# Performance work log

Hardware: AMD Instinct MI355X
Metric: run time of the kernel (lower is better)

## Reference

```python
import jax, jax.numpy as jnp
import numpy as np

B, E, H, W, HEADS = 2, 128, 64, 64, 4
FUSED = 2 * E + 1          # concat fusion: C_state + C_trigger + 1 (gnn context)
FC = FUSED // 2            # 128 fusion output channels (= AttentionMIL feature_dim)
EPS = 1e-5
NEG = -1e9


def _conv(x, w, b=None, pad=0):
    out = jax.lax.conv_general_dilated(x, w, (1, 1), [(pad, pad), (pad, pad)],
                                       dimension_numbers=('NCHW', 'OIHW', 'NCHW'))
    return out if b is None else out + b[None, :, None, None]


def _bn(x, g, b):
    # training-mode batchnorm (batch statistics), matching torch default mode
    m = x.mean((0, 2, 3), keepdims=True)
    v = x.var((0, 2, 3), keepdims=True)
    return g[None, :, None, None] * (x - m) * jax.lax.rsqrt(v + EPS) + b[None, :, None, None]


def _mha(q_in, kv_in, w_qkv, b_qkv, w_out, b_out, nheads):
    Bq, L, Em = q_in.shape
    d = Em // nheads
    wq, wk, wv = jnp.split(w_qkv, 3, axis=0)
    bq, bk, bv = jnp.split(b_qkv, 3, axis=0)
    q = (q_in @ wq.T + bq).reshape(Bq, L, nheads, d)
    k = (kv_in @ wk.T + bk).reshape(Bq, -1, nheads, d)
    v = (kv_in @ wv.T + bv).reshape(Bq, -1, nheads, d)
    scores = jnp.einsum('bqhd,bkhd->bhqk', q, k) / jnp.sqrt(jnp.asarray(d, q.dtype))
    attn = jax.nn.softmax(scores, axis=-1)
    out = jnp.einsum('bhqk,bkhd->bqhd', attn, v).reshape(Bq, L, Em)
    return out @ w_out.T + b_out


def setup_inputs() -> dict:
    key = jax.random.key(0)
    ks = jax.random.split(key, 24)
    n = lambda k, s: jax.random.normal(k, s, jnp.float32)
    p = lambda k, s: 0.02 * jax.random.normal(k, s, jnp.float32)
    return dict(
        state_features=n(ks[0], (B, E, H, W)),
        trigger_features=n(ks[1], (B, E, H, W)),
        gnn_context=n(ks[2], (B, 1, H, W)),
        zone_patches=jax.random.randint(ks[3], (B, H, W), 0, 16).astype(jnp.int32),
        cats=jax.random.randint(ks[4], (B,), 0, 16).astype(jnp.int32),
        labels=jax.random.uniform(ks[5], (B,), jnp.float32),
        s2t_qkv_w=p(ks[6], (3 * E, E)), s2t_qkv_b=p(ks[7], (3 * E,)),
        s2t_out_w=p(ks[8], (E, E)), s2t_out_b=p(ks[9], (E,)),
        t2s_qkv_w=p(ks[10], (3 * E, E)), t2s_qkv_b=p(ks[11], (3 * E,)),
        t2s_out_w=p(ks[12], (E, E)), t2s_out_b=p(ks[13], (E,)),
        fconv1_w=p(ks[14], (FC, FUSED, 3, 3)),
        fbn1_g=jnp.ones((FC,), jnp.float32), fbn1_b=jnp.zeros((FC,), jnp.float32),
        fconv2_w=p(ks[15], (FC, FC, 3, 3)),
        fbn2_g=jnp.ones((FC,), jnp.float32), fbn2_b=jnp.zeros((FC,), jnp.float32),
        outc_w=p(ks[16], (1, FC, 1, 1)), outc_b=p(ks[17], (1,)),
        attn1_w=p(ks[18], (128, FC, 1, 1)), attn1_b=p(ks[19], (128,)),
        attn2_w=p(ks[20], (1, 128, 1, 1)), attn2_b=p(ks[21], (1,)),
    )


def reference(state_features, trigger_features, gnn_context, zone_patches, cats, labels,
              s2t_qkv_w, s2t_qkv_b, s2t_out_w, s2t_out_b,
              t2s_qkv_w, t2s_qkv_b, t2s_out_w, t2s_out_b,
              fconv1_w, fbn1_g, fbn1_b, fconv2_w, fbn2_g, fbn2_b,
              outc_w, outc_b, attn1_w, attn1_b, attn2_w, attn2_b):
    Bs = state_features.shape[0]
    # ---- CrossAttentionFusion ----
    sf = state_features.reshape(Bs, E, H * W).transpose(0, 2, 1)    # (B, HW, E)
    tf = trigger_features.reshape(Bs, E, H * W).transpose(0, 2, 1)
    s2t = _mha(sf, tf, s2t_qkv_w, s2t_qkv_b, s2t_out_w, s2t_out_b, HEADS)
    t2s = _mha(tf, sf, t2s_qkv_w, t2s_qkv_b, t2s_out_w, t2s_out_b, HEADS)
    s2t = s2t.transpose(0, 2, 1).reshape(Bs, E, H, W)
    t2s = t2s.transpose(0, 2, 1).reshape(Bs, E, H, W)
    fused = jnp.concatenate([s2t, t2s, gnn_context], axis=1)        # (B, 257, H, W)
    x = jax.nn.relu(_bn(_conv(fused, fconv1_w, pad=1), fbn1_g, fbn1_b))
    feat = jax.nn.relu(_bn(_conv(x, fconv2_w, pad=1), fbn2_g, fbn2_b))  # (B, FC, H, W)
    # ---- pixel logit head (decoder outc) ----
    pixel_logits = _conv(feat, outc_w, outc_b)[:, 0]                # (B, H, W)
    # ---- AttentionMIL (vectorized over batch) ----
    a = jax.nn.relu(_conv(feat, attn1_w, attn1_b))
    scores = _conv(a, attn2_w, attn2_b)[:, 0]                       # (B, H, W)
    mask = (zone_patches == cats[:, None, None]) & (zone_patches > 0)
    has = mask.any((1, 2))
    masked = jnp.where(mask, scores, NEG)                           # score*1 on valid, -1e9 elsewhere
    wts = jax.nn.softmax(masked.reshape(Bs, -1), axis=-1).reshape(Bs, H, W)
    attention_maps = jnp.where(has[:, None, None], wts, 0.0)
    bag = (pixel_logits * wts * mask.astype(wts.dtype)).sum((1, 2))
    bag = jnp.where(has, bag, 0.0)
    # BCEWithLogitsLoss(mean): softplus(x) - x*y
    loss = jnp.mean(jax.nn.softplus(bag) - bag * labels)
    return loss, attention_maps
```

## Files before the change

kernel.cpp:

```cpp
#include <hip/hip_runtime.h>
#include <hip/hip_bf16.h>
#include <math.h>

#define L 4096
#define ECH 128
#define BCH 2
#define NHEAD 4
#define FUSEDC 257
#define CPAD 288

typedef __attribute__((ext_vector_type(8))) short bs8;
typedef __attribute__((ext_vector_type(4))) short bs4;
typedef __attribute__((ext_vector_type(4))) float fx4;

#define SCL 0.25503518f

static __device__ __forceinline__ short f2bfs(float x) {
  unsigned u = __float_as_uint(x);
  u += 0x7fffu + ((u >> 16) & 1u);
  return (short)(u >> 16);
}

static __device__ __forceinline__ float bf2f(short s) {
  return __uint_as_float((unsigned)(unsigned short)s << 16);
}

static __device__ __forceinline__ float exp2a(float x) {
  float r; asm("v_exp_f32 %0, %1" : "=v"(r) : "v"(x)); return r;
}

static __device__ __forceinline__ unsigned pk2(float lo, float hi) {
  unsigned r; asm("v_cvt_pk_bf16_f32 %0, %1, %2" : "=v"(r) : "v"(lo), "v"(hi)); return r;
}

__global__ void prep_fused(const float* __restrict__ c1w, const float* __restrict__ c2w,
                           const float* __restrict__ wS, const float* __restrict__ wT,
                           const float* __restrict__ woS, const float* __restrict__ woT,
                           const float* __restrict__ sf, const float* __restrict__ tf,
                           short* __restrict__ W1b, short* __restrict__ W2b,
                           short* __restrict__ wSb, short* __restrict__ wTb,
                           short* __restrict__ woSb, short* __restrict__ woTb,
                           short* __restrict__ Xs, short* __restrict__ Xt) {
  __shared__ float t[32][33];
  int bid = blockIdx.x;
  if (bid < 2064) {
    int i = bid * 256 + threadIdx.x;
    if (i < 331776) {
      int ci = i % CPAD; int rest = i / CPAD; int co = rest & 127; int tap = rest >> 7;
      W1b[i] = (ci < FUSEDC) ? f2bfs(c1w[(co * FUSEDC + ci) * 9 + tap]) : (short)0;
    } else if (i < 479232) {
      int j = i - 331776;
      int ci = j & 127; int co = (j >> 7) & 127; int tap = j >> 14;
      W2b[j] = f2bfs(c2w[(co * 128 + ci) * 9 + tap]);
    } else {
      int k = i - 479232;
      float s = (k < 16384) ? SCL : 1.0f;
      wSb[k] = f2bfs(wS[k] * s);
      wTb[k] = f2bfs(wT[k] * s);
      if (k < 16384) {
        woSb[k] = f2bfs(woS[k]);
        woTb[k] = f2bfs(woT[k]);
      }
    }
  } else {
    int id = bid - 2064;
    int bx = (id & 127) * 32;
    int by = ((id >> 7) & 3) * 32;
    int z = id >> 9; int b = z & 1; int sel = z >> 1;
    const float* in = sel ? tf : sf;
    short* out = sel ? Xt : Xs;
    int tx = threadIdx.x & 31, ty = threadIdx.x >> 5;
    const float* ip = in + (size_t)b * ECH * L;
    short* op = out + (size_t)b * L * ECH;
#pragma unroll
    for (int r = ty; r < 32; r += 8)
      t[r][tx] = ip[(size_t)(by + r) * L + bx + tx];
    __syncthreads();
#pragma unroll
    for (int r = ty; r < 32; r += 8)
      op[(size_t)(bx + r) * ECH + by + tx] = f2bfs(t[tx][r]);
  }
}

__global__ void __launch_bounds__(256)
gemm_qkv(const short* __restrict__ Xs, const short* __restrict__ Xt,
         const short* __restrict__ wSb, const short* __restrict__ wTb,
         const float* __restrict__ bS, const float* __restrict__ bT,
         short* __restrict__ qs, short* __restrict__ ks,
         short* __restrict__ qt, short* __restrict__ kt,
         short* __restrict__ vTs, short* __restrict__ vTt) {
  int unit = blockIdx.y;
  const short* X; const short* W; const float* bias; short* out; float scale; int mode;
  switch (unit) {
    case 0: X = Xs; W = wSb;         bias = bS;       out = qs;  scale = SCL; mode = 0; break;
    case 1: X = Xt; W = wSb + 16384; bias = bS + 128; out = ks;  scale = 1.f; mode = 1; break;
    case 2: X = Xt; W = wTb;         bias = bT;       out = qt;  scale = SCL; mode = 0; break;
    case 3: X = Xs; W = wTb + 16384; bias = bT + 128; out = kt;  scale = 1.f; mode = 1; break;
    case 4: X = Xt; W = wSb + 32768; bias = bS + 256; out = vTs; scale = 1.f; mode = 2; break;
    default:X = Xs; W = wTb + 32768; bias = bT + 256; out = vTt; scale = 1.f; mode = 2; break;
  }
  int tid = threadIdx.x;
  int wv = tid >> 6, lane = tid & 63, u = lane >> 4, r = lane & 15;
  int pblk = blockIdx.x * 64 + wv * 16;
  const short* xrow = X + (size_t)(pblk + r) * 128;
  fx4 acc[8] = {};
  if (mode != 2) {
#pragma unroll
    for (int ksx = 0; ksx < 4; ++ksx) {
      int k0 = ksx * 32 + u * 8;
      bs8 a = *(const bs8*)(xrow + k0);
      const short* wp = W + (size_t)r * 128 + k0;
#pragma unroll
      for (int t = 0; t < 8; ++t) {
        bs8 wf = *(const bs8*)(wp + (size_t)t * 16 * 128);
        acc[t] = __builtin_amdgcn_mfma_f32_16x16x32_bf16(a, wf, acc[t], 0, 0, 0);
      }
    }
  } else {
#pragma unroll
    for (int ksx = 0; ksx < 4; ++ksx) {
      int k0 = ksx * 32 + u * 8;
      bs8 xb = *(const bs8*)(xrow + k0);
      const short* wp = W + (size_t)r * 128 + k0;
#pragma unroll
      for (int t = 0; t < 8; ++t) {
        bs8 wf = *(const bs8*)(wp + (size_t)t * 16 * 128);
        acc[t] = __builtin_amdgcn_mfma_f32_16x16x32_bf16(wf, xb, acc[t], 0, 0, 0);
      }
    }
  }
  if (mode == 0) {
#pragma unroll
    for (int t = 0; t < 8; ++t) {
      float bv = bias[t * 16 + r] * scale;
#pragma unroll
      for (int reg = 0; reg < 4; ++reg) {
        int p = pblk + u * 4 + reg;
        out[(size_t)p * 128 + t * 16 + r] = f2bfs(acc[t][reg] + bv);
      }
    }
  } else if (mode == 1) {
#pragma unroll
    for (int t = 0; t < 8; ++t) {
      int och = t * 16 + r, h = och >> 5, d = och & 31;
      float bv = bias[och];
#pragma unroll
      for (int reg = 0; reg < 4; ++reg) {
        int p = pblk + u * 4 + reg;
        int b = p >> 12, pl = p & 4095;
        out[(((size_t)(b * NHEAD + h) * L + pl) << 5) + d] = f2bfs(acc[t][reg] + bv);
      }
    }
  } else {
    int p = pblk + r;
    int b = p >> 12, pl = p & 4095;
#pragma unroll
    for (int t = 0; t < 8; ++t) {
#pragma unroll
      for (int reg = 0; reg < 4; ++reg) {
        int och = t * 16 + u * 4 + reg;
        int h = och >> 5, d = och & 31;
        out[((size_t)(b * NHEAD + h) * 32 + d) * L + pl] = f2bfs(acc[t][reg] + bias[och]);
      }
    }
  }
}

__global__ void __launch_bounds__(256)
gemm_o(const short* __restrict__ aosb, const short* __restrict__ aotb,
       const short* __restrict__ woSb, const short* __restrict__ woTb,
       const float* __restrict__ boS, const float* __restrict__ boT,
       const float* __restrict__ gnn, short* __restrict__ fusedPM) {
  int unit = blockIdx.y;
  const short* X = unit ? aotb : aosb;
  const short* W = unit ? woTb : woSb;
  const float* bias = unit ? boT : boS;
  int ochbase = unit ? 128 : 0;
  int tid = threadIdx.x;
  int wv = tid >> 6, lane = tid & 63, u = lane >> 4, r = lane & 15;
  int pblk = blockIdx.x * 64 + wv * 16;
  const short* xrow = X + (size_t)(pblk + r) * 128;
  fx4 acc[8] = {};
#pragma unroll
  for (int ksx = 0; ksx < 4; ++ksx) {
    int k0 = ksx * 32 + u * 8;
    bs8 a = *(const bs8*)(xrow + k0);
    const short* wp = W + (size_t)r * 128 + k0;
#pragma unroll
    for (int t = 0; t < 8; ++t) {
      bs8 wf = *(const bs8*)(wp + (size_t)t * 16 * 128);
      acc[t] = __builtin_amdgcn_mfma_f32_16x16x32_bf16(a, wf, acc[t], 0, 0, 0);
    }
  }
#pragma unroll
  for (int t = 0; t < 8; ++t) {
    float bv = bias[t * 16 + r];
#pragma unroll
    for (int reg = 0; reg < 4; ++reg) {
      int p = pblk + u * 4 + reg;
      fusedPM[(size_t)p * CPAD + ochbase + t * 16 + r] = f2bfs(acc[t][reg] + bv);
    }
  }
  if (unit == 0) {
    int base = blockIdx.x * 64;
    for (int t2 = tid; t2 < 64 * 32; t2 += 256) {
      int p = base + (t2 >> 5), j = t2 & 31;
      fusedPM[(size_t)p * CPAD + 256 + j] = (j == 0) ? f2bfs(gnn[p]) : (short)0;
    }
  }
}

__global__ void __launch_bounds__(256, 4)
flash_attn6(const short* __restrict__ Qs, const short* __restrict__ Ks, const short* __restrict__ Vs,
            const short* __restrict__ Qt, const short* __restrict__ Kt, const short* __restrict__ Vt,
            short* __restrict__ poS, short* __restrict__ poT,
            float* __restrict__ pmS, float* __restrict__ plS,
            float* __restrict__ pmT, float* __restrict__ plT) {
  int z = blockIdx.z;
  int sp = z >> 2, att = (z >> 1) & 1, b = z & 1;
  const short* Q = att ? Qt : Qs;
  const short* K = att ? Kt : Ks;
  const short* VT = att ? Vt : Vs;
  short* po = att ? poT : poS;
  float* pm = att ? pmT : pmS;
  float* pl = att ? plT : plS;
  int tid = threadIdx.x;
  int wid = tid >> 6, lane = tid & 63;
  int u = lane >> 4, r = lane & 15;
  int h = blockIdx.y;
  int qt0 = (blockIdx.x << 4) + (wid << 2);
  bs8 qf0 = *(const bs8*)(Q + ((size_t)(b * L + ((qt0 + 0) << 4) + r) * 128 + h * 32 + u * 8));
  bs8 qf1 = *(const bs8*)(Q + ((size_t)(b * L + ((qt0 + 1) << 4) + r) * 128 + h * 32 + u * 8));
  bs8 qf2 = *(const bs8*)(Q + ((size_t)(b * L + ((qt0 + 2) << 4) + r) * 128 + h * 32 + u * 8));
  bs8 qf3 = *(const bs8*)(Q + ((size_t)(b * L + ((qt0 + 3) << 4) + r) * 128 + h * 32 + u * 8));
  const short* Kb = K + (((size_t)(b * NHEAD + h) * L + sp * 1024) << 5) + u * 8;
  const short* Vb = VT + ((size_t)(b * NHEAD + h) * 32) * (size_t)L + sp * 1024;
  const short* v0p = Vb + (size_t)r * L + (u << 2);
  const short* v1p = Vb + (size_t)(16 + r) * L + (u << 2);
  fx4 o0[4] = {}, o1[4] = {};
  float l[4] = {0.f, 0.f, 0.f, 0.f};
  float m = -1.0e30f;
#pragma unroll 1
  for (int k0 = 0; k0 < 1024; k0 += 64) {
    bs8 a0 = *(const bs8*)(Kb + (((size_t)(k0 + r)) << 5));
    bs8 a1 = *(const bs8*)(Kb + (((size_t)(k0 + 16 + r)) << 5));
    bs8 a2 = *(const bs8*)(Kb + (((size_t)(k0 + 32 + r)) << 5));
    bs8 a3 = *(const bs8*)(Kb + (((size_t)(k0 + 48 + r)) << 5));
    bs4 w0 = *(const bs4*)(v0p + k0);
    bs4 w1 = *(const bs4*)(v0p + k0 + 16);
    bs4 w2 = *(const bs4*)(v0p + k0 + 32);
    bs4 w3 = *(const bs4*)(v0p + k0 + 48);
    bs4 w4 = *(const bs4*)(v1p + k0);
    bs4 w5 = *(const bs4*)(v1p + k0 + 16);
    bs4 w6 = *(const bs4*)(v1p + k0 + 32);
    bs4 w7 = *(const bs4*)(v1p + k0 + 48);
    bs8 vb0lo = __builtin_shufflevector(w0, w1, 0, 1, 2, 3, 4, 5, 6, 7);
    bs8 vb0hi = __builtin_shufflevector(w2, w3, 0, 1, 2, 3, 4, 5, 6, 7);
    bs8 vb1lo = __builtin_shufflevector(w4, w5, 0, 1, 2, 3, 4, 5, 6, 7);
    bs8 vb1hi = __builtin_shufflevector(w6, w7, 0, 1, 2, 3, 4, 5, 6, 7);
    fx4 zz = {0.f, 0.f, 0.f, 0.f};
#pragma unroll
    for (int t = 0; t < 4; ++t) {
      bs8 qf = (t == 0) ? qf0 : (t == 1) ? qf1 : (t == 2) ? qf2 : qf3;
      fx4 s0 = __builtin_amdgcn_mfma_f32_16x16x32_bf16(a0, qf, zz, 0, 0, 0);
      fx4 s1 = __builtin_amdgcn_mfma_f32_16x16x32_bf16(a1, qf, zz, 0, 0, 0);
      fx4 s2 = __builtin_amdgcn_mfma_f32_16x16x32_bf16(a2, qf, zz, 0, 0, 0);
      fx4 s3 = __builtin_amdgcn_mfma_f32_16x16x32_bf16(a3, qf, zz, 0, 0, 0);
      float mx = fmaxf(fmaxf(fmaxf(s0[0], s0[1]), fmaxf(s0[2], s0[3])),
                       fmaxf(fmaxf(s1[0], s1[1]), fmaxf(s1[2], s1[3])));
      mx = fmaxf(mx, fmaxf(fmaxf(fmaxf(s2[0], s2[1]), fmaxf(s2[2], s2[3])),
                           fmaxf(fmaxf(s3[0], s3[1]), fmaxf(s3[2], s3[3]))));
      if (!__all(mx <= m + 8.0f)) {
        float gm = fmaxf(mx, __shfl_xor(mx, 1));
        gm = fmaxf(gm, __shfl_xor(gm, 2));
        gm = fmaxf(gm, __shfl_xor(gm, 4));
        gm = fmaxf(gm, __shfl_xor(gm, 8));
        gm = fmaxf(gm, __shfl_xor(gm, 16));
        gm = fmaxf(gm, __shfl_xor(gm, 32));
        float m_new = fmaxf(m, gm);
        float fsc = exp2a(m - m_new);
#pragma unroll
        for (int tt = 0; tt < 4; ++tt) {
          l[tt] *= fsc;
#pragma unroll
          for (int rg = 0; rg < 4; ++rg) { o0[tt][rg] *= fsc; o1[tt][rg] *= fsc; }
        }
        m = m_new;
      }
      fx4 p0, p1, p2, p3;
#pragma unroll
      for (int i = 0; i < 4; ++i) {
        p0[i] = exp2a(s0[i] - m);
        p1[i] = exp2a(s1[i] - m);
        p2[i] = exp2a(s2[i] - m);
        p3[i] = exp2a(s3[i] - m);
      }
      l[t] += ((p0[0] + p0[1]) + (p0[2] + p0[3])) + ((p1[0] + p1[1]) + (p1[2] + p1[3]))
            + ((p2[0] + p2[1]) + (p2[2] + p2[3])) + ((p3[0] + p3[1]) + (p3[2] + p3[3]));
      union { unsigned w32[4]; bs8 v; } plo, phi;
      plo.w32[0] = pk2(p0[0], p0[1]); plo.w32[1] = pk2(p0[2], p0[3]);
      plo.w32[2] = pk2(p1[0], p1[1]); plo.w32[3] = pk2(p1[2], p1[3]);
      phi.w32[0] = pk2(p2[0], p2[1]); phi.w32[1] = pk2(p2[2], p2[3]);
      phi.w32[2] = pk2(p3[0], p3[1]); phi.w32[3] = pk2(p3[2], p3[3]);
      o0[t] = __builtin_amdgcn_mfma_f32_16x16x32_bf16(plo.v, vb0lo, o0[t], 0, 0, 0);
      o0[t] = __builtin_amdgcn_mfma_f32_16x16x32_bf16(phi.v, vb0hi, o0[t], 0, 0, 0);
      o1[t] = __builtin_amdgcn_mfma_f32_16x16x32_bf16(plo.v, vb1lo, o1[t], 0, 0, 0);
      o1[t] = __builtin_amdgcn_mfma_f32_16x16x32_bf16(phi.v, vb1hi, o1[t], 0, 0, 0);
    }
  }
#pragma unroll
  for (int t = 0; t < 4; ++t) {
    float lt = l[t];
    lt += __shfl_xor(lt, 16);
    lt += __shfl_xor(lt, 32);
    int rowb = ((b * NHEAD + h) << 12) + ((qt0 + t) << 4);
    if (lane < 16) {
      pm[(sp << 15) + rowb + r] = m;
      pl[(sp << 15) + rowb + r] = lt;
    }
#pragma unroll
    for (int reg = 0; reg < 4; ++reg) {
      size_t ob = ((size_t)sp << 20) + ((size_t)(rowb + (u << 2) + reg) << 5);
      po[ob + r] = f2bfs(o0[t][reg]);
      po[ob + 16 + r] = f2bfs(o1[t][reg]);
    }
  }
}

__global__ void combine_attn(const short* __restrict__ poS, const float* __restrict__ pmS,
                             const float* __restrict__ plS,
                             const short* __restrict__ poT, const float* __restrict__ pmT,
                             const float* __restrict__ plT,
                             short* __restrict__ aos, short* __restrict__ aot) {
  int i = blockIdx.x * 256 + threadIdx.x;
  int att = i >> 20, j = i & 0xFFFFF;
  const short* po = att ? poT : poS;
  const float* pm = att ? pmT : pmS;
  const float* pl = att ? plT : plS;
  short* out = att ? aot : aos;
  int row = j >> 5, d = j & 31;
  float m0 = pm[row], m1 = pm[32768 + row];
  float m2 = pm[65536 + row], m3 = pm[98304 + row];
  float l0 = pl[row], l1 = pl[32768 + row];
  float l2 = pl[65536 + row], l3 = pl[98304 + row];
  float m = fmaxf(fmaxf(m0, m1), fmaxf(m2, m3));
  float f0 = exp2f(m0 - m), f1 = exp2f(m1 - m);
  float f2 = exp2f(m2 - m), f3 = exp2f(m3 - m);
  float v0 = bf2f(po[j]);
  float v1 = bf2f(po[(1 << 20) + j]);
  float v2 = bf2f(po[(2 << 20) + j]);
  float v3 = bf2f(po[(3 << 20) + j]);
  float num = v0 * f0 + v1 * f1 + v2 * f2 + v3 * f3;
  float den = l0 * f0 + l1 * f1 + l2 * f2 + l3 * f3;
  float val = num / den;
  int q = row & 4095, h = (row >> 12) & 3, b = row >> 14;
  out[(((size_t)(b << 12) + q) << 7) + (h << 5) + d] = f2bfs(val);
}

__global__ void __launch_bounds__(128)
conv1_mfma(const short* __restrict__ X, const short* __restrict__ W,
           float* __restrict__ out, float* __restrict__ psum, float* __restrict__ psq) {
  int tid = threadIdx.x;
  int wv = tid >> 6, lane = tid & 63, u = lane >> 4, r = lane & 15;
  int pblk = blockIdx.x * 32 + wv * 16;
  int ybase = blockIdx.y * 32;
  int b = pblk >> 12, y = (pblk & 4095) >> 6, x0 = pblk & 63;
  fx4 acc[2] = {};
  for (int tap = 0; tap < 9; ++tap) {
    int dy = tap / 3 - 1, dx = tap % 3 - 1;
    int yy = y + dy;
    if (yy < 0 || yy > 63) { __syncthreads(); continue; }
    int xx = x0 + r + dx;
    bool valid = (xx >= 0) && (xx <= 63);
    const short* xrow = X + (size_t)((b << 12) + (yy << 6) + x0 + dx + r) * CPAD;
    const short* wtap = W + ((size_t)tap * 128 + ybase + r) * CPAD;
#pragma unroll
    for (int kc = 0; kc < 9; ++kc) {
      int k0 = kc * 32 + u * 8;
      bs8 a = {};
      if (valid) a = *(const bs8*)(xrow + k0);
#pragma unroll
      for (int t = 0; t < 2; ++t) {
        bs8 wf = *(const bs8*)(wtap + (size_t)t * 16 * CPAD + k0);
        acc[t] = __builtin_amdgcn_mfma_f32_16x16x32_bf16(a, wf, acc[t], 0, 0, 0);
      }
    }
    __syncthreads();
  }
#pragma unroll
  for (int t = 0; t < 2; ++t) {
#pragma unroll
    for (int reg = 0; reg < 4; ++reg)
      out[(size_t)(pblk + u * 4 + reg) * 128 + ybase + t * 16 + r] = acc[t][reg];
    float s = (acc[t][0] + acc[t][1]) + (acc[t][2] + acc[t][3]);
    float q = (acc[t][0] * acc[t][0] + acc[t][1] * acc[t][1])
            + (acc[t][2] * acc[t][2] + acc[t][3] * acc[t][3]);
    s += __shfl_xor(s, 16); s += __shfl_xor(s, 32);
    q += __shfl_xor(q, 16); q += __shfl_xor(q, 32);
    if (u == 0) {
      int slot = (ybase + t * 16 + r) * 512 + blockIdx.x * 2 + wv;
      psum[slot] = s;
      psq[slot] = q;
    }
  }
}

__global__ void __launch_bounds__(128)
conv2_mfma(const short* __restrict__ X, const short* __restrict__ W,
           float* __restrict__ out, float* __restrict__ psum, float* __restrict__ psq) {
  int tid = threadIdx.x;
  int wv = tid >> 6, lane = tid & 63, u = lane >> 4, r = lane & 15;
  int pblk = blockIdx.x * 32 + wv * 16;
  int ybase = blockIdx.y * 32;
  int b = pblk >> 12, y = (pblk & 4095) >> 6, x0 = pblk & 63;
  fx4 acc[2] = {};
  for (int tap = 0; tap < 9; ++tap) {
    int dy = tap / 3 - 1, dx = tap % 3 - 1;
    int yy = y + dy;
    if (yy < 0 || yy > 63) { __syncthreads(); continue; }
    int xx = x0 + r + dx;
    bool valid = (xx >= 0) && (xx <= 63);
    const short* xrow = X + (size_t)((b << 12) + (yy << 6) + x0 + dx + r) * 128;
    const short* wtap = W + ((size_t)tap * 128 + ybase + r) * 128;
#pragma unroll
    for (int kc = 0; kc < 4; ++kc) {
      int k0 = kc * 32 + u * 8;
      bs8 xb = {};
      if (valid) xb = *(const bs8*)(xrow + k0);
#pragma unroll
      for (int t = 0; t < 2; ++t) {
        bs8 wf = *(const bs8*)(wtap + (size_t)t * 16 * 128 + k0);
        acc[t] = __builtin_amdgcn_mfma_f32_16x16x32_bf16(wf, xb, acc[t], 0, 0, 0);
      }
    }
    __syncthreads();
  }
  int px = y * 64 + x0 + r;
#pragma unroll
  for (int t = 0; t < 2; ++t) {
#pragma unroll
    for (int reg = 0; reg < 4; ++reg) {
      int och = ybase + t * 16 + u * 4 + reg;
      out[((size_t)(b * 128 + och) << 12) + px] = acc[t][reg];
    }
#pragma unroll
    for (int reg = 0; reg < 4; ++reg) {
      float s = acc[t][reg];
      float q = s * s;
      s += __shfl_xor(s, 1); q += __shfl_xor(q, 1);
      s += __shfl_xor(s, 2); q += __shfl_xor(q, 2);
      s += __shfl_xor(s, 4); q += __shfl_xor(q, 4);
      s += __shfl_xor(s, 8); q += __shfl_xor(q, 8);
      if (r == 0) {
        int slot = (ybase + t * 16 + u * 4 + reg) * 512 + blockIdx.x * 2 + wv;
        psum[slot] = s;
        psq[slot] = q;
      }
    }
  }
}

__global__ void stats_reduce(const float* __restrict__ psum, const float* __restrict__ psq,
                             float* __restrict__ mean, float* __restrict__ rstd) {
  __shared__ float rs[256], rq[256];
  int c = blockIdx.x, tid = threadIdx.x;
  float s = psum[c * 512 + tid] + psum[c * 512 + 256 + tid];
  float q = psq[c * 512 + tid] + psq[c * 512 + 256 + tid];
  rs[tid] = s; rq[tid] = q; __syncthreads();
  for (int st = 128; st > 0; st >>= 1) {
    if (tid < st) { rs[tid] += rs[tid + st]; rq[tid] += rq[tid + st]; }
    __syncthreads();
  }
  if (tid == 0) {
    float m = rs[0] / 8192.0f;
    float v = rq[0] / 8192.0f - m * m;
    mean[c] = m;
    rstd[c] = rsqrtf(v + 1e-5f);
  }
}

__global__ void bnapply_pm(const float* __restrict__ x, const float* __restrict__ mean,
                           const float* __restrict__ rstd, const float* __restrict__ g,
                           const float* __restrict__ bb, short* __restrict__ out) {
  int i = blockIdx.x * 256 + threadIdx.x;
  int c = i & 127;
  float v = x[i];
  out[i] = f2bfs(fmaxf(g[c] * (v - mean[c]) * rstd[c] + bb[c], 0.0f));
}

__global__ void head_kernel(const float* __restrict__ feat,
                            const float* __restrict__ bmean, const float* __restrict__ brstd,
                            const float* __restrict__ bg, const float* __restrict__ bbias,
                            const float* __restrict__ w1, const float* __restrict__ b1,
                            const float* __restrict__ w2, const float* __restrict__ b2,
                            const float* __restrict__ wo, const float* __restrict__ bo,
                            float* __restrict__ score, float* __restrict__ plog) {
  __shared__ float f[128][64];
  __shared__ float r1[4][64], r2[4][64];
  int by = blockIdx.x; int b = by >> 6, y = by & 63;
  int tid = threadIdx.x;
  int x = tid & 63, g4 = tid >> 6;
  for (int c = g4; c < 128; c += 4) {
    float v = feat[((size_t)(b * 128 + c)) * L + y * 64 + x];
    f[c][x] = fmaxf(bg[c] * (v - bmean[c]) * brstd[c] + bbias[c], 0.0f);
  }
  __syncthreads();
  int cb = g4 * 32;
  float a[32];
#pragma unroll
  for (int i = 0; i < 32; ++i) a[i] = b1[cb + i];
  for (int ci = 0; ci < 128; ++ci) {
    float fv = f[ci][x];
#pragma unroll
    for (int i = 0; i < 32; ++i) a[i] += w1[(size_t)(cb + i) * 128 + ci] * fv;
  }
  float sp = 0.0f;
#pragma unroll
  for (int i = 0; i < 32; ++i) sp += w2[cb + i] * fmaxf(a[i], 0.0f);
  float plp = 0.0f;
#pragma unroll
  for (int i = 0; i < 32; ++i) plp += wo[cb + i] * f[cb + i][x];
  r1[g4][x] = sp; r2[g4][x] = plp;
  __syncthreads();
  if (tid < 64) {
    int xx = tid;
    float s = r1[0][xx] + r1[1][xx] + r1[2][xx] + r1[3][xx] + b2[0];
    float pl = r2[0][xx] + r2[1][xx] + r2[2][xx] + r2[3][xx] + bo[0];
    score[(size_t)b * L + y * 64 + xx] = s;
    plog[(size_t)b * L + y * 64 + xx] = pl;
  }
}

__global__ void finalize_kernel(const float* __restrict__ score, const float* __restrict__ plog,
                                const int* __restrict__ zone, const int* __restrict__ cats,
                                float* __restrict__ maps, float* __restrict__ bag_ws) {
  __shared__ float sc[4096];
  __shared__ float red[256];
  __shared__ int ired[256];
  int b = blockIdx.x, tid = threadIdx.x;
  int cat = cats[b];
  float lmax = -3e38f; int lhas = 0;
  for (int p = tid; p < 4096; p += 256) {
    int z = zone[(size_t)b * 4096 + p];
    int m = (z == cat) && (z > 0);
    float s = m ? score[(size_t)b * 4096 + p] : -1e9f;
    sc[p] = s; lmax = fmaxf(lmax, s); lhas |= m;
  }
  red[tid] = lmax; ired[tid] = lhas; __syncthreads();
  for (int st = 128; st > 0; st >>= 1) {
    if (tid < st) { red[tid] = fmaxf(red[tid], red[tid + st]); ired[tid] |= ired[tid + st]; }
    __syncthreads();
  }
  float gmax = red[0]; int has = ired[0];
  __syncthreads();
  float lsum = 0;
  for (int p = tid; p < 4096; p += 256) {
    float e = __expf(sc[p] - gmax);
    sc[p] = e; lsum += e;
  }
  red[tid] = lsum; __syncthreads();
  for (int st = 128; st > 0; st >>= 1) { if (tid < st) red[tid] += red[tid + st]; __syncthreads(); }
  float inv = 1.0f / red[0];
  __syncthreads();
  float lbag = 0;
  for (int p = tid; p < 4096; p += 256) {
    float w = sc[p] * inv;
    maps[(size_t)b * 4096 + p] = has ? w : 0.0f;
    int z = zone[(size_t)b * 4096 + p];
    if ((z == cat) && (z > 0)) lbag += plog[(size_t)b * 4096 + p] * w;
  }
  red[tid] = lbag; __syncthreads();
  for (int st = 128; st > 0; st >>= 1) { if (tid < st) red[tid] += red[tid + st]; __syncthreads(); }
  if (tid == 0) bag_ws[b] = has ? red[0] : 0.0f;
}

__global__ void loss_kernel(const float* __restrict__ bag_ws, const float* __restrict__ labels,
                            float* __restrict__ out) {
  if (threadIdx.x == 0 && blockIdx.x == 0) {
    float t = 0;
    for (int b = 0; b < BCH; ++b) {
      float x = bag_ws[b];
      float sp = fmaxf(x, 0.0f) + log1pf(expf(-fabsf(x)));
      t += sp - x * labels[b];
    }
    out[0] = t / (float)BCH;
  }
}

extern "C" void kernel_launch(void* const* d_in, const int* in_sizes, int n_in,
                              void* d_out, int out_size, void* d_ws, size_t ws_size,
                              hipStream_t stream) {
  (void)in_sizes; (void)n_in; (void)out_size; (void)ws_size;
  const float* state = (const float*)d_in[0];
  const float* trig  = (const float*)d_in[1];
  const float* gnn   = (const float*)d_in[2];
  const int*   zone  = (const int*)d_in[3];
  const int*   cats  = (const int*)d_in[4];
  const float* labels = (const float*)d_in[5];
  const float* s2t_qkv_w = (const float*)d_in[6];
  const float* s2t_qkv_b = (const float*)d_in[7];
  const float* s2t_out_w = (const float*)d_in[8];
  const float* s2t_out_b = (const float*)d_in[9];
  const float* t2s_qkv_w = (const float*)d_in[10];
  const float* t2s_qkv_b = (const float*)d_in[11];
  const float* t2s_out_w = (const float*)d_in[12];
  const float* t2s_out_b = (const float*)d_in[13];
  const float* fconv1_w = (const float*)d_in[14];
  const float* fbn1_g = (const float*)d_in[15];
  const float* fbn1_b = (const float*)d_in[16];
  const float* fconv2_w = (const float*)d_in[17];
  const float* fbn2_g = (const float*)d_in[18];
  const float* fbn2_b = (const float*)d_in[19];
  const float* outc_w = (const float*)d_in[20];
  const float* outc_b = (const float*)d_in[21];
  const float* attn1_w = (const float*)d_in[22];
  const float* attn1_b = (const float*)d_in[23];
  const float* attn2_w = (const float*)d_in[24];
  const float* attn2_b = (const float*)d_in[25];

  float* ws = (float*)d_ws;
  const size_t NBP = (size_t)BCH * L * 128;
  size_t o = 0;
  float* c1 = ws + o; o += NBP;
  float* c2 = ws + o; o += NBP;
  float* stats = ws + o; o += 512;
  float* score = ws + o; o += (size_t)BCH * L;
  float* plog = ws + o; o += (size_t)BCH * L;
  float* bag = ws + o; o += 8;
  short* Xs = (short*)(ws + o); o += NBP / 2;
  short* Xt = (short*)(ws + o); o += NBP / 2;
  short* qsb = (short*)(ws + o); o += NBP / 2;
  short* ksb = (short*)(ws + o); o += NBP / 2;
  short* qtb = (short*)(ws + o); o += NBP / 2;
  short* ktb = (short*)(ws + o); o += NBP / 2;
  short* vTsb = (short*)(ws + o); o += NBP / 2;
  short* vTtb = (short*)(ws + o); o += NBP / 2;
  short* aosb = (short*)(ws + o); o += NBP / 2;
  short* aotb = (short*)(ws + o); o += NBP / 2;
  short* fusedPM = (short*)(ws + o); o += (size_t)BCH * L * CPAD / 2;
  short* X2 = (short*)(ws + o); o += NBP / 2;
  short* W1b = (short*)(ws + o); o += (9 * 128 * CPAD) / 2;
  short* W2b = (short*)(ws + o); o += (9 * 128 * 128) / 2;
  short* wSb = (short*)(ws + o); o += 24576;
  short* wTb = (short*)(ws + o); o += 24576;
  short* woSb = (short*)(ws + o); o += 8192;
  short* woTb = (short*)(ws + o); o += 8192;
  short* poT = (short*)(ws + o); o += 2 * NBP;
  float* psum1 = ws + o; o += 128 * 512;
  float* psq1 = ws + o; o += 128 * 512;
  float* psum2 = ws + o; o += 128 * 512;
  float* psq2 = ws + o; o += 128 * 512;

  short* poS = (short*)c1;
  float* pmS = (float*)fusedPM;
  float* plS = pmS + 131072;
  float* pmT = plS + 131072;
  float* plT = pmT + 131072;

  prep_fused<<<4112, 256, 0, stream>>>(fconv1_w, fconv2_w, s2t_qkv_w, t2s_qkv_w,
                                       s2t_out_w, t2s_out_w, state, trig,
                                       W1b, W2b, wSb, wTb, woSb, woTb, Xs, Xt);

  gemm_qkv<<<dim3(128, 6), 256, 0, stream>>>(Xs, Xt, wSb, wTb, s2t_qkv_b, t2s_qkv_b,
                                             qsb, ksb, qtb, ktb, vTsb, vTtb);

  flash_attn6<<<dim3(16, NHEAD, 16), 256, 0, stream>>>(qsb, ksb, vTsb, qtb, ktb, vTtb,
                                                       poS, poT, pmS, plS, pmT, plT);
  combine_attn<<<8192, 256, 0, stream>>>(poS, pmS, plS, poT, pmT, plT, aosb, aotb);

  gemm_o<<<dim3(128, 2), 256, 0, stream>>>(aosb, aotb, woSb, woTb, s2t_out_b, t2s_out_b,
                                           gnn, fusedPM);

  conv1_mfma<<<dim3(256, 4), 128, 0, stream>>>(fusedPM, W1b, c1, psum1, psq1);
  stats_reduce<<<128, 256, 0, stream>>>(psum1, psq1, stats, stats + 128);
  bnapply_pm<<<4096, 256, 0, stream>>>(c1, stats, stats + 128, fbn1_g, fbn1_b, X2);

  conv2_mfma<<<dim3(256, 4), 128, 0, stream>>>(X2, W2b, c2, psum2, psq2);
  stats_reduce<<<128, 256, 0, stream>>>(psum2, psq2, stats + 256, stats + 384);

  head_kernel<<<BCH * 64, 256, 0, stream>>>(c2, stats + 256, stats + 384, fbn2_g, fbn2_b,
                                            attn1_w, attn1_b, attn2_w, attn2_b,
                                            outc_w, outc_b, score, plog);

  finalize_kernel<<<BCH, 256, 0, stream>>>(score, plog, zone, cats, (float*)d_out + 1, bag);
  loss_kernel<<<1, 64, 0, stream>>>(bag, labels, (float*)d_out);
}
```

Before: 255.5 us.

## Fuse split-K attention combine into output projection GEMM and add MFMA priority hints

Removes the separate combine_attn kernel. The output-projection GEMM now reads the four split-K partial attention outputs with their max and sum statistics, rescales and normalises them in registers, and feeds them straight into the MFMA. This drops one kernel launch and a bf16 intermediate round trip through memory. The partial-statistics buffers move to X2 and a new workspace area, so they no longer alias fusedPM, which gemm_o now writes. s_setprio hints are also wrapped around the MFMA groups in flash attention.

New measurement: 250.0 us (median of 2 runs). 1.02x faster.

```diff
diff --git a/kernel.cpp b/kernel.cpp
--- a/kernel.cpp
+++ b/kernel.cpp
@@ -167,29 +167,53 @@
 }
 
 __global__ void __launch_bounds__(256)
-gemm_o(const short* __restrict__ aosb, const short* __restrict__ aotb,
+gemm_o(const short* __restrict__ poS, const float* __restrict__ pmS, const float* __restrict__ plS,
+       const short* __restrict__ poT, const float* __restrict__ pmT, const float* __restrict__ plT,
        const short* __restrict__ woSb, const short* __restrict__ woTb,
        const float* __restrict__ boS, const float* __restrict__ boT,
        const float* __restrict__ gnn, short* __restrict__ fusedPM) {
   int unit = blockIdx.y;
-  const short* X = unit ? aotb : aosb;
+  const short* po = unit ? poT : poS;
+  const float* pm = unit ? pmT : pmS;
+  const float* pl = unit ? plT : plS;
   const short* W = unit ? woTb : woSb;
   const float* bias = unit ? boT : boS;
   int ochbase = unit ? 128 : 0;
   int tid = threadIdx.x;
   int wv = tid >> 6, lane = tid & 63, u = lane >> 4, r = lane & 15;
   int pblk = blockIdx.x * 64 + wv * 16;
-  const short* xrow = X + (size_t)(pblk + r) * 128;
+  int p = pblk + r, bb = p >> 12, q = p & 4095;
   fx4 acc[8] = {};
 #pragma unroll
   for (int ksx = 0; ksx < 4; ++ksx) {
-    int k0 = ksx * 32 + u * 8;
-    bs8 a = *(const bs8*)(xrow + k0);
-    const short* wp = W + (size_t)r * 128 + k0;
+    int row = ((bb * NHEAD + ksx) << 12) + q;
+    float m0 = pm[row], m1 = pm[32768 + row];
+    float m2 = pm[65536 + row], m3 = pm[98304 + row];
+    float l0 = pl[row], l1 = pl[32768 + row];
+    float l2 = pl[65536 + row], l3 = pl[98304 + row];
+    float mm = fmaxf(fmaxf(m0, m1), fmaxf(m2, m3));
+    float f0 = exp2a(m0 - mm), f1 = exp2a(m1 - mm);
+    float f2 = exp2a(m2 - mm), f3 = exp2a(m3 - mm);
+    float inv = 1.0f / (l0 * f0 + l1 * f1 + l2 * f2 + l3 * f3);
+    int base = (row << 5) + u * 8;
+    bs8 v0 = *(const bs8*)(po + base);
+    bs8 v1 = *(const bs8*)(po + (1 << 20) + base);
+    bs8 v2 = *(const bs8*)(po + (2 << 20) + base);
+    bs8 v3 = *(const bs8*)(po + (3 << 20) + base);
+    union { unsigned w32[4]; bs8 v; } pa;
+#pragma unroll
+    for (int jj = 0; jj < 4; ++jj) {
+      float lo = (bf2f(v0[2 * jj]) * f0 + bf2f(v1[2 * jj]) * f1
+                + bf2f(v2[2 * jj]) * f2 + bf2f(v3[2 * jj]) * f3) * inv;
+      float hi = (bf2f(v0[2 * jj + 1]) * f0 + bf2f(v1[2 * jj + 1]) * f1
+                + bf2f(v2[2 * jj + 1]) * f2 + bf2f(v3[2 * jj + 1]) * f3) * inv;
+      pa.w32[jj] = pk2(lo, hi);
+    }
+    const short* wp = W + (size_t)r * 128 + ksx * 32 + u * 8;
 #pragma unroll
     for (int t = 0; t < 8; ++t) {
       bs8 wf = *(const bs8*)(wp + (size_t)t * 16 * 128);
-      acc[t] = __builtin_amdgcn_mfma_f32_16x16x32_bf16(a, wf, acc[t], 0, 0, 0);
+      acc[t] = __builtin_amdgcn_mfma_f32_16x16x32_bf16(pa.v, wf, acc[t], 0, 0, 0);
     }
   }
 #pragma unroll
@@ -197,15 +221,15 @@
     float bv = bias[t * 16 + r];
 #pragma unroll
     for (int reg = 0; reg < 4; ++reg) {
-      int p = pblk + u * 4 + reg;
-      fusedPM[(size_t)p * CPAD + ochbase + t * 16 + r] = f2bfs(acc[t][reg] + bv);
+      int pp = pblk + u * 4 + reg;
+      fusedPM[(size_t)pp * CPAD + ochbase + t * 16 + r] = f2bfs(acc[t][reg] + bv);
     }
   }
   if (unit == 0) {
     int base = blockIdx.x * 64;
     for (int t2 = tid; t2 < 64 * 32; t2 += 256) {
-      int p = base + (t2 >> 5), j = t2 & 31;
-      fusedPM[(size_t)p * CPAD + 256 + j] = (j == 0) ? f2bfs(gnn[p]) : (short)0;
+      int pp = base + (t2 >> 5), j = t2 & 31;
+      fusedPM[(size_t)pp * CPAD + 256 + j] = (j == 0) ? f2bfs(gnn[pp]) : (short)0;
     }
   }
 }
@@ -262,10 +286,12 @@
 #pragma unroll
     for (int t = 0; t < 4; ++t) {
       bs8 qf = (t == 0) ? qf0 : (t == 1) ? qf1 : (t == 2) ? qf2 : qf3;
+      __builtin_amdgcn_s_setprio(1);
       fx4 s0 = __builtin_amdgcn_mfma_f32_16x16x32_bf16(a0, qf, zz, 0, 0, 0);
       fx4 s1 = __builtin_amdgcn_mfma_f32_16x16x32_bf16(a1, qf, zz, 0, 0, 0);
       fx4 s2 = __builtin_amdgcn_mfma_f32_16x16x32_bf16(a2, qf, zz, 0, 0, 0);
       fx4 s3 = __builtin_amdgcn_mfma_f32_16x16x32_bf16(a3, qf, zz, 0, 0, 0);
+      __builtin_amdgcn_s_setprio(0);
       float mx = fmaxf(fmaxf(fmaxf(s0[0], s0[1]), fmaxf(s0[2], s0[3])),
                        fmaxf(fmaxf(s1[0], s1[1]), fmaxf(s1[2], s1[3])));
       mx = fmaxf(mx, fmaxf(fmaxf(fmaxf(s2[0], s2[1]), fmaxf(s2[2], s2[3])),
@@ -302,10 +328,12 @@
       plo.w32[2] = pk2(p1[0], p1[1]); plo.w32[3] = pk2(p1[2], p1[3]);
       phi.w32[0] = pk2(p2[0], p2[1]); phi.w32[1] = pk2(p2[2], p2[3]);
       phi.w32[2] = pk2(p3[0], p3[1]); phi.w32[3] = pk2(p3[2], p3[3]);
+      __builtin_amdgcn_s_setprio(1);
       o0[t] = __builtin_amdgcn_mfma_f32_16x16x32_bf16(plo.v, vb0lo, o0[t], 0, 0, 0);
       o0[t] = __builtin_amdgcn_mfma_f32_16x16x32_bf16(phi.v, vb0hi, o0[t], 0, 0, 0);
       o1[t] = __builtin_amdgcn_mfma_f32_16x16x32_bf16(plo.v, vb1lo, o1[t], 0, 0, 0);
       o1[t] = __builtin_amdgcn_mfma_f32_16x16x32_bf16(phi.v, vb1hi, o1[t], 0, 0, 0);
+      __builtin_amdgcn_s_setprio(0);
     }
   }
 #pragma unroll
@@ -325,36 +353,6 @@
       po[ob + 16 + r] = f2bfs(o1[t][reg]);
     }
   }
-}
-
-__global__ void combine_attn(const short* __restrict__ poS, const float* __restrict__ pmS,
-                             const float* __restrict__ plS,
-                             const short* __restrict__ poT, const float* __restrict__ pmT,
-                             const float* __restrict__ plT,
-                             short* __restrict__ aos, short* __restrict__ aot) {
-  int i = blockIdx.x * 256 + threadIdx.x;
-  int att = i >> 20, j = i & 0xFFFFF;
-  const short* po = att ? poT : poS;
-  const float* pm = att ? pmT : pmS;
-  const float* pl = att ? plT : plS;
-  short* out = att ? aot : aos;
-  int row = j >> 5, d = j & 31;
-  float m0 = pm[row], m1 = pm[32768 + row];
-  float m2 = pm[65536 + row], m3 = pm[98304 + row];
-  float l0 = pl[row], l1 = pl[32768 + row];
-  float l2 = pl[65536 + row], l3 = pl[98304 + row];
-  float m = fmaxf(fmaxf(m0, m1), fmaxf(m2, m3));
-  float f0 = exp2f(m0 - m), f1 = exp2f(m1 - m);
-  float f2 = exp2f(m2 - m), f3 = exp2f(m3 - m);
-  float v0 = bf2f(po[j]);
-  float v1 = bf2f(po[(1 << 20) + j]);
-  float v2 = bf2f(po[(2 << 20) + j]);
-  float v3 = bf2f(po[(3 << 20) + j]);
-  float num = v0 * f0 + v1 * f1 + v2 * f2 + v3 * f3;
-  float den = l0 * f0 + l1 * f1 + l2 * f2 + l3 * f3;
-  float val = num / den;
-  int q = row & 4095, h = (row >> 12) & 3, b = row >> 14;
-  out[(((size_t)(b << 12) + q) << 7) + (h << 5) + d] = f2bfs(val);
 }
 
 __global__ void __launch_bounds__(128)
@@ -635,8 +633,6 @@
   short* ktb = (short*)(ws + o); o += NBP / 2;
   short* vTsb = (short*)(ws + o); o += NBP / 2;
   short* vTtb = (short*)(ws + o); o += NBP / 2;
-  short* aosb = (short*)(ws + o); o += NBP / 2;
-  short* aotb = (short*)(ws + o); o += NBP / 2;
   short* fusedPM = (short*)(ws + o); o += (size_t)BCH * L * CPAD / 2;
   short* X2 = (short*)(ws + o); o += NBP / 2;
   short* W1b = (short*)(ws + o); o += (9 * 128 * CPAD) / 2;
@@ -650,12 +646,14 @@
   float* psq1 = ws + o; o += 128 * 512;
   float* psum2 = ws + o; o += 128 * 512;
   float* psq2 = ws + o; o += 128 * 512;
+  float* pmT2 = ws + o; o += 4 * 32768;
+  float* plT2 = ws + o; o += 4 * 32768;
 
   short* poS = (short*)c1;
-  float* pmS = (float*)fusedPM;
+  float* pmS = (float*)X2;
   float* plS = pmS + 131072;
-  float* pmT = plS + 131072;
-  float* plT = pmT + 131072;
+  float* pmT = pmT2;
+  float* plT = plT2;
 
   prep_fused<<<4112, 256, 0, stream>>>(fconv1_w, fconv2_w, s2t_qkv_w, t2s_qkv_w,
                                        s2t_out_w, t2s_out_w, state, trig,
@@ -666,9 +664,9 @@
 
   flash_attn6<<<dim3(16, NHEAD, 16), 256, 0, stream>>>(qsb, ksb, vTsb, qtb, ktb, vTtb,
                                                        poS, poT, pmS, plS, pmT, plT);
-  combine_attn<<<8192, 256, 0, stream>>>(poS, pmS, plS, poT, pmT, plT, aosb, aotb);
-
-  gemm_o<<<dim3(128, 2), 256, 0, stream>>>(aosb, aotb, woSb, woTb, s2t_out_b, t2s_out_b,
+
+  gemm_o<<<dim3(128, 2), 256, 0, stream>>>(poS, pmS, plS, poT, pmT, plT,
+                                           woSb, woTb, s2t_out_b, t2s_out_b,
                                            gnn, fusedPM);
 
   conv1_mfma<<<dim3(256, 4), 128, 0, stream>>>(fusedPM, W1b, c1, psum1, psq1);
```
